# Performance work log

Hardware: AMD Instinct MI355X
Metric: run time of the kernel (lower is better)

## Reference

```python
import jax, jax.numpy as jnp
import numpy as np

HEADS = 8
EPS = 1e-5


def setup_inputs() -> dict:
    key = jax.random.key(0)
    ks = jax.random.split(key, 9)
    B, C, H, W = 4, 256, 128, 128
    s1 = 0.02
    inp = {
        "fmap": jax.random.normal(ks[0], (B, C, H, W), dtype=jnp.float32),
        "g": jnp.ones((C, 1, 1), dtype=jnp.float32),
        "wq1": jax.random.normal(ks[1], (C, C, 1, 1), dtype=jnp.float32) * s1,
        "wq2": jax.random.normal(ks[2], (C, 1, 3, 3), dtype=jnp.float32) * s1,
        "wk1": jax.random.normal(ks[3], (C, C, 1, 1), dtype=jnp.float32) * s1,
        "wk2": jax.random.normal(ks[4], (C, 1, 3, 3), dtype=jnp.float32) * s1,
        "wv1": jax.random.normal(ks[5], (C, C, 1, 1), dtype=jnp.float32) * s1,
        "wv2": jax.random.normal(ks[6], (C, 1, 3, 3), dtype=jnp.float32) * s1,
        "w_out": jax.random.normal(ks[7], (C, C, 1, 1), dtype=jnp.float32) * s1,
    }
    return inp


def _linear_attention(fmap, g, wq1, wq2, wk1, wk2, wv1, wv2, w_out):
    b, C, H, W = fmap.shape
    h = HEADS
    c = C // h          # head dim
    n = H * W           # tokens
    scale = c ** -0.5

    # channel LayerNorm over dim=-3 (C), learned gamma, no bias
    mean = jnp.mean(fmap, axis=1, keepdims=True)
    var = jnp.var(fmap, axis=1, keepdims=True)
    x = (fmap - mean) * jax.lax.rsqrt(var + EPS) * g[None]

    def proj(w1, w2):
        # 1x1 conv (no bias) then 3x3 depthwise conv (groups=C), SAME pad
        y = jnp.einsum('bchw,oc->bohw', x, w1[:, :, 0, 0])
        return jax.lax.conv_general_dilated(
            y, w2, window_strides=(1, 1), padding='SAME',
            dimension_numbers=('NCHW', 'OIHW', 'NCHW'),
            feature_group_count=C)

    q, k, v = proj(wq1, wq2), proj(wk1, wk2), proj(wv1, wv2)

    def to_heads(t):  # [b,C,H,W] -> [b*h, n, c]
        return t.reshape(b, h, c, n).transpose(0, 1, 3, 2).reshape(b * h, n, c)

    q, k, v = to_heads(q), to_heads(k), to_heads(v)

    q = jax.nn.softmax(q, axis=-1) * scale   # softmax over head dim
    k = jax.nn.softmax(k, axis=-2)            # softmax over tokens

    ctx = jnp.einsum('bnd,bne->bde', k, v)    # [b*h, c, c]
    out = jnp.einsum('bnd,bde->bne', q, ctx)  # [b*h, n, c]

    out = out.reshape(b, h, n, c).transpose(0, 1, 3, 2).reshape(b, C, H, W)
    out = jax.nn.silu(out)
    return jnp.einsum('bchw,oc->bohw', out, w_out[:, :, 0, 0])


def reference(fmap, g, wq1, wq2, wk1, wk2, wv1, wv2, w_out):
    return _linear_attention(fmap, g, wq1, wq2, wk1, wk2, wv1, wv2, w_out)
```

## Files before the change

kernel.cpp:

```cpp
#include <hip/hip_runtime.h>
#include <cmath>


#define B 4
#define C 256
#define Hh 128
#define Wd 128
#define HW (Hh*Wd)
#define HEADS 8
#define HD 32
#define OSCALE 256.0f
#define NSP 16

typedef _Float16 half_t;
typedef _Float16 f16x8 __attribute__((ext_vector_type(8)));
typedef float f32x4 __attribute__((ext_vector_type(4)));

__device__ __forceinline__ void gload_lds16(const half_t* g, half_t* l) {
  __builtin_amdgcn_global_load_lds((const __attribute__((address_space(1))) void*)g,
                                   (__attribute__((address_space(3))) void*)l, 16, 0, 0);
}

__global__ __launch_bounds__(256) void wcvt_all(const float* __restrict__ wq1,
                                                const float* __restrict__ wk1,
                                                const float* __restrict__ wv1,
                                                const float* __restrict__ wout,
                                                half_t* __restrict__ Wh,
                                                half_t* __restrict__ Woh,
                                                float* __restrict__ Sk) {
  int i = blockIdx.x * 256 + threadIdx.x;
  if (i < 65536) Wh[i] = (half_t)wq1[i];
  else if (i < 131072) Wh[i] = (half_t)wk1[i - 65536];
  else if (i < 196608) Wh[i] = (half_t)wv1[i - 131072];
  else Woh[i - 196608] = (half_t)wout[i - 196608];
  if (i < B * C) Sk[i] = 0.f;
}

__global__ __launch_bounds__(256) void ln2(const float* __restrict__ fmap,
                                           const float* __restrict__ g,
                                           half_t* __restrict__ Xh) {
  int b = blockIdx.y;
  int lane = threadIdx.x & 63;
  int gq = threadIdx.x >> 6;
  int px = blockIdx.x * 64 + lane;
  __shared__ float gs[C];
  __shared__ float sm1[4][64], sm2[4][64];
  gs[threadIdx.x] = g[threadIdx.x];
  const float* fp = fmap + ((size_t)b * C + gq * 64) * HW + px;
  float vbuf[64];
  float s = 0.f, s2 = 0.f;
#pragma unroll
  for (int j = 0; j < 64; ++j) {
    float v = fp[(size_t)j * HW];
    vbuf[j] = v;
    s += v; s2 = fmaf(v, v, s2);
  }
  sm1[gq][lane] = s; sm2[gq][lane] = s2;
  __syncthreads();
  float st = 0.f, st2 = 0.f;
#pragma unroll
  for (int q = 0; q < 4; ++q) { st += sm1[q][lane]; st2 += sm2[q][lane]; }
  float mean = st * (1.f / C);
  float var = st2 * (1.f / C) - mean * mean;
  float rstd = rsqrtf(var + 1e-5f);
  half_t* xp = Xh + ((size_t)b * HW + px) * 256 + gq * 64;
#pragma unroll
  for (int j0 = 0; j0 < 64; j0 += 8) {
    f16x8 v8;
#pragma unroll
    for (int jj = 0; jj < 8; ++jj)
      v8[jj] = (half_t)((vbuf[j0 + jj] - mean) * rstd * gs[gq * 64 + j0 + jj]);
    *(f16x8*)(xp + j0) = v8;
  }
}

__global__ __launch_bounds__(512) void gemm16r(const half_t* __restrict__ Xh,
                                               const half_t* __restrict__ Wh,
                                               half_t* __restrict__ Yh) {
  __shared__ __align__(16) char smem[65536];
  const int tid = threadIdx.x;
  const int wave = tid >> 6, lane = tid & 63;
  const int lr = lane & 15, lq = lane >> 4;
  const int b = blockIdx.z;
  const int pix0 = blockIdx.x * 128;
  const int m0 = blockIdx.y * 128;
  const int wm = wave >> 1, wn = wave & 1;

  const half_t* xb = Xh + ((size_t)b * HW + pix0) * 256;
  const half_t* wb = Wh + (size_t)m0 * 256;

  f32x4 acc[2][4];
#pragma unroll
  for (int i = 0; i < 2; ++i)
#pragma unroll
    for (int j = 0; j < 4; ++j) { f32x4 z = {0.f, 0.f, 0.f, 0.f}; acc[i][j] = z; }

#define STAGE(kt, s) do {                                                       \
    int r_ = tid >> 2, c_ = tid & 3;                                            \
    int cs_ = c_ ^ ((r_ >> 1) & 3);                                             \
    gload_lds16(xb + (size_t)r_ * 256 + (kt) * 32 + (cs_ << 3),                 \
                (half_t*)(smem + (s) * 16384) + tid * 8);                       \
    gload_lds16(wb + (size_t)r_ * 256 + (kt) * 32 + (cs_ << 3),                 \
                (half_t*)(smem + (s) * 16384 + 8192) + tid * 8);                \
  } while (0)

  STAGE(0, 0);
  STAGE(1, 1);

#pragma unroll
  for (int t = 0; t < 8; ++t) {
    if (t < 6) STAGE(t + 2, (t + 2) & 3);
    if (t < 6)       asm volatile("s_waitcnt vmcnt(4)" ::: "memory");
    else if (t == 6) asm volatile("s_waitcnt vmcnt(2)" ::: "memory");
    else             asm volatile("s_waitcnt vmcnt(0)" ::: "memory");
    __builtin_amdgcn_sched_barrier(0);
    __builtin_amdgcn_s_barrier();
    const char* slot = smem + (t & 3) * 16384;
    f16x8 afr[2], bfr[4];
#pragma unroll
    for (int mf = 0; mf < 2; ++mf) {
      int r = wm * 32 + mf * 16 + lr;
      afr[mf] = *(const f16x8*)(slot + 8192 + r * 64 + ((lq ^ ((r >> 1) & 3)) << 4));
    }
#pragma unroll
    for (int nf = 0; nf < 4; ++nf) {
      int r = wn * 64 + nf * 16 + lr;
      bfr[nf] = *(const f16x8*)(slot + r * 64 + ((lq ^ ((r >> 1) & 3)) << 4));
    }
#pragma unroll
    for (int mf = 0; mf < 2; ++mf)
#pragma unroll
      for (int nf = 0; nf < 4; ++nf)
        acc[mf][nf] = __builtin_amdgcn_mfma_f32_16x16x32_f16(afr[mf], bfr[nf], acc[mf][nf], 0, 0, 0);
  }
#undef STAGE
  asm volatile("s_waitcnt lgkmcnt(0)" ::: "memory");
  __builtin_amdgcn_sched_barrier(0);
  __builtin_amdgcn_s_barrier();

#pragma unroll
  for (int mf = 0; mf < 2; ++mf)
#pragma unroll
    for (int nf = 0; nf < 4; ++nf)
#pragma unroll
      for (int j = 0; j < 4; ++j) {
        int row = wm * 32 + mf * 16 + lq * 4 + j;
        int col = wn * 64 + nf * 16 + lr;
        int byte = row * 256 + ((col * 2) ^ ((row & 7) << 4));
        *(half_t*)(smem + byte) = (half_t)acc[mf][nf][j];
      }
  __syncthreads();
  half_t* dst_base = Yh + (size_t)(m0 >> 8) * ((size_t)B * C * HW)
                     + ((size_t)(b * C + (m0 & 255))) * HW + pix0;
#pragma unroll
  for (int it = 0; it < 4; ++it) {
    int i = it * 512 + tid;
    int row = i >> 4, ch = i & 15;
    int src = row * 256 + ((ch * 16) ^ ((row & 7) << 4));
    *(f16x8*)(dst_base + (size_t)row * HW + ch * 8) = *(const f16x8*)(smem + src);
  }
}

__global__ __launch_bounds__(256) void dw3x3_all(const half_t* __restrict__ Yh,
                                                 const float* __restrict__ wq2,
                                                 const float* __restrict__ wk2,
                                                 const float* __restrict__ wv2,
                                                 half_t* __restrict__ Qh,
                                                 half_t* __restrict__ EK,
                                                 half_t* __restrict__ Vh,
                                                 float* __restrict__ Sk) {
  const size_t SZ = (size_t)B * C * HW;
  int ch = blockIdx.y;
  int ten = ch >> 8;
  int c = ch & 255;
  int b = blockIdx.z;
  int r = threadIdx.x >> 4;
  int cg = threadIdx.x & 15;
  int lane = threadIdx.x & 63;
  int j0 = cg * 8;
  int i = blockIdx.x * 16 + r;
  const half_t* plane = Yh + (size_t)ten * SZ + ((size_t)(b * C + c)) * HW;
  const float* W2 = (ten == 0) ? wq2 : (ten == 1) ? wk2 : wv2;
  half_t wh[9];
#pragma unroll
  for (int k = 0; k < 9; ++k) wh[k] = (half_t)W2[c * 9 + k];
  const int lm1 = (lane - 1) & 63, lp1 = (lane + 1) & 63;
  f16x8 acc8 = {0, 0, 0, 0, 0, 0, 0, 0};
#pragma unroll
  for (int dr = 0; dr < 3; ++dr) {
    int ii = i + dr - 1;
    if (ii < 0 || ii >= Hh) continue;
    uint4 d = *(const uint4*)(plane + ii * Wd + j0);
    unsigned haloL = (unsigned)__shfl((int)d.w, lm1);
    unsigned haloR = (unsigned)__shfl((int)d.x, lp1);
    if (cg == 0)  haloL = 0;
    if (cg == 15) haloR = 0;
    unsigned m0 = __builtin_amdgcn_alignbit(d.x, haloL, 16);
    unsigned m1 = __builtin_amdgcn_alignbit(d.y, d.x, 16);
    unsigned m2 = __builtin_amdgcn_alignbit(d.z, d.y, 16);
    unsigned m3 = __builtin_amdgcn_alignbit(d.w, d.z, 16);
    unsigned m4 = __builtin_amdgcn_alignbit(haloR, d.w, 16);
    uint4 lshu = {m0, m1, m2, m3};
    uint4 rshu = {m1, m2, m3, m4};
    f16x8 cv  = __builtin_bit_cast(f16x8, d);
    f16x8 lsh = __builtin_bit_cast(f16x8, lshu);
    f16x8 rsh = __builtin_bit_cast(f16x8, rshu);
    acc8 += lsh * wh[dr * 3] + cv * wh[dr * 3 + 1] + rsh * wh[dr * 3 + 2];
  }
  size_t off = ((size_t)(b * C + c)) * HW + i * Wd + j0;
  if (ten == 1) {
    f16x8 o8;
    float local = 0.f;
#pragma unroll
    for (int p = 0; p < 8; ++p) {
      float e = expf((float)acc8[p]);
      o8[p] = (half_t)e;
      local += e;
    }
    *(f16x8*)(EK + off) = o8;
    __shared__ float red[256];
    int t = threadIdx.x;
    red[t] = local; __syncthreads();
    for (int st = 128; st > 0; st >>= 1) {
      if (t < st) red[t] += red[t + st];
      __syncthreads();
    }
    if (t == 0) atomicAdd(&Sk[b * C + c], red[0]);
  } else {
    half_t* dst = (ten == 0) ? Qh : Vh;
    *(f16x8*)(dst + off) = acc8;
  }
}

__global__ __launch_bounds__(256) void ctx_mfma(const half_t* __restrict__ EK,
                                                const half_t* __restrict__ V,
                                                float* __restrict__ part) {
  int bh = blockIdx.x, sp = blockIdx.y;
  int wave = threadIdx.x >> 6, lane = threadIdx.x & 63;
  int lr = lane & 15, lq = lane >> 4;
  const size_t base = (size_t)bh * HD * HW;
  const half_t* ekp = EK + base + (size_t)lr * HW;
  const half_t* vp  = V  + base + (size_t)lr * HW;
  f32x4 a00 = {0.f,0.f,0.f,0.f}, a01 = a00, a10 = a00, a11 = a00;
  const int n0w = sp * 1024 + wave * 256 + lq * 8;
#pragma unroll
  for (int ks = 0; ks < 8; ++ks) {
    int n = n0w + ks * 32;
    f16x8 fa0 = *(const f16x8*)(ekp + n);
    f16x8 fa1 = *(const f16x8*)(ekp + (size_t)16 * HW + n);
    f16x8 fb0 = *(const f16x8*)(vp + n);
    f16x8 fb1 = *(const f16x8*)(vp + (size_t)16 * HW + n);
    a00 = __builtin_amdgcn_mfma_f32_16x16x32_f16(fa0, fb0, a00, 0, 0, 0);
    a01 = __builtin_amdgcn_mfma_f32_16x16x32_f16(fa0, fb1, a01, 0, 0, 0);
    a10 = __builtin_amdgcn_mfma_f32_16x16x32_f16(fa1, fb0, a10, 0, 0, 0);
    a11 = __builtin_amdgcn_mfma_f32_16x16x32_f16(fa1, fb1, a11, 0, 0, 0);
  }
  __shared__ float red[4][1024];
#pragma unroll
  for (int j = 0; j < 4; ++j) {
    int dlo = lq * 4 + j;
    red[wave][(dlo)      * 32 + lr]      = a00[j];
    red[wave][(dlo)      * 32 + 16 + lr] = a01[j];
    red[wave][(dlo + 16) * 32 + lr]      = a10[j];
    red[wave][(dlo + 16) * 32 + 16 + lr] = a11[j];
  }
  __syncthreads();
  float* pp = part + ((size_t)sp * 32 + bh) * 1024;
  for (int idx = threadIdx.x; idx < 1024; idx += 256)
    pp[idx] = red[0][idx] + red[1][idx] + red[2][idx] + red[3][idx];
}

__global__ __launch_bounds__(256) void ctxred(const float* __restrict__ part,
                                              const float* __restrict__ Sk,
                                              half_t* __restrict__ ctxh) {
  int bh = blockIdx.x;
  int t = threadIdx.x;
  for (int idx = t; idx < 1024; idx += 256) {
    int d = idx >> 5, e = idx & 31;
    float s = 0.f;
#pragma unroll
    for (int sp = 0; sp < NSP; ++sp) s += part[((size_t)sp * 32 + bh) * 1024 + idx];
    ctxh[(size_t)bh * 1024 + e * 32 + d] = (half_t)(s / Sk[bh * HD + d]);
  }
}

__global__ __launch_bounds__(256) void attn6b(const half_t* __restrict__ Qh,
                                              const half_t* __restrict__ ctxh,
                                              const half_t* __restrict__ Woh,
                                              float* __restrict__ outp) {
  const int b = blockIdx.y;
  const int lane = threadIdx.x & 63;
  const int w = threadIdx.x >> 6;
  const int lr = lane & 15, lq = lane >> 4;
  const int px0 = blockIdx.x * 64;
  const int px = px0 + w * 16 + lr;
  __shared__ __align__(16) char osm[64 * 512];

  {
    const int pxl_base = w * 16 + lq * 4;
    const half_t* cb = ctxh + ((size_t)b * HEADS) * 1024;
    f16x8 cf0 = *(const f16x8*)(cb + (lr)      * 32 + lq * 8);
    f16x8 cf1 = *(const f16x8*)(cb + (16 + lr) * 32 + lq * 8);
#pragma unroll
    for (int h = 0; h < HEADS; ++h) {
      f16x8 nf0, nf1;
      if (h < HEADS - 1) {
        const half_t* nb = cb + (size_t)(h + 1) * 1024;
        nf0 = *(const f16x8*)(nb + (lr)      * 32 + lq * 8);
        nf1 = *(const f16x8*)(nb + (16 + lr) * 32 + lq * 8);
      }
      const half_t* qp = Qh + ((size_t)(b * C + h * HD + lq * 8)) * HW + px;
      float ev[8];
      float psum = 0.f;
#pragma unroll
      for (int j = 0; j < 8; ++j) {
        ev[j] = expf((float)qp[(size_t)j * HW]);
        psum += ev[j];
      }
      float s = psum;
      s += __shfl_xor(s, 16, 64);
      s += __shfl_xor(s, 32, 64);
      float inv = 0.1767766952966369f / s;
      f16x8 pa;
#pragma unroll
      for (int j = 0; j < 8; ++j) pa[j] = (half_t)(ev[j] * inv);

      f32x4 z = {0.f, 0.f, 0.f, 0.f};
      f32x4 a0 = __builtin_amdgcn_mfma_f32_16x16x32_f16(pa, cf0, z, 0, 0, 0);
      f32x4 a1 = __builtin_amdgcn_mfma_f32_16x16x32_f16(pa, cf1, z, 0, 0, 0);
#pragma unroll
      for (int eh = 0; eh < 2; ++eh) {
        f32x4 a = eh ? a1 : a0;
        int cc = h * 32 + eh * 16 + lr;
#pragma unroll
        for (int j = 0; j < 4; ++j) {
          int pxl = pxl_base + j;
          float v = a[j];
          float sg = 1.f / (1.f + expf(-v));
          int byte = pxl * 512 + ((cc * 2) ^ ((pxl & 7) << 4));
          *(half_t*)(osm + byte) = (half_t)(v * sg * OSCALE);
        }
      }
      cf0 = nf0; cf1 = nf1;
    }
  }
  __syncthreads();

  f32x4 acc[4][4];
#pragma unroll
  for (int i = 0; i < 4; ++i)
#pragma unroll
    for (int j = 0; j < 4; ++j) { f32x4 z = {0.f, 0.f, 0.f, 0.f}; acc[i][j] = z; }

  const half_t* wbase = Woh + ((size_t)(w * 64 + lr)) * 256 + lq * 8;
#pragma unroll
  for (int k0 = 0; k0 < 256; k0 += 32) {
    f16x8 afr[4], bfr[4];
#pragma unroll
    for (int mf = 0; mf < 4; ++mf)
      afr[mf] = *(const f16x8*)(wbase + (size_t)(mf * 16) * 256 + k0);
#pragma unroll
    for (int nf = 0; nf < 4; ++nf) {
      int r = nf * 16 + lr;
      bfr[nf] = *(const f16x8*)(osm + r * 512 + ((k0 * 2 + lq * 16) ^ ((r & 7) << 4)));
    }
#pragma unroll
    for (int mf = 0; mf < 4; ++mf)
#pragma unroll
      for (int nf = 0; nf < 4; ++nf)
        acc[mf][nf] = __builtin_amdgcn_mfma_f32_16x16x32_f16(afr[mf], bfr[nf], acc[mf][nf], 0, 0, 0);
  }

#pragma unroll
  for (int mf = 0; mf < 4; ++mf) {
    int oc = w * 64 + mf * 16 + lq * 4;
#pragma unroll
    for (int nf = 0; nf < 4; ++nf) {
      float* dst = outp + ((size_t)(b * C + oc)) * HW + px0 + nf * 16 + lr;
#pragma unroll
      for (int j = 0; j < 4; ++j)
        dst[(size_t)j * HW] = acc[mf][nf][j] * (1.0f / OSCALE);
    }
  }
}

extern "C" void kernel_launch(void* const* d_in, const int* in_sizes, int n_in,
                              void* d_out, int out_size, void* d_ws, size_t ws_size,
                              hipStream_t stream) {
  const float* fmap = (const float*)d_in[0];
  const float* g    = (const float*)d_in[1];
  const float* wq1  = (const float*)d_in[2];
  const float* wq2  = (const float*)d_in[3];
  const float* wk1  = (const float*)d_in[4];
  const float* wk2  = (const float*)d_in[5];
  const float* wv1  = (const float*)d_in[6];
  const float* wv2  = (const float*)d_in[7];
  const float* wout = (const float*)d_in[8];
  float* out = (float*)d_out;
  char* ws = (char*)d_ws;

  const size_t SZ = (size_t)B * C * HW;
  const size_t Mi = (size_t)1 << 20;
  half_t* Xh   = (half_t*)(ws);
  half_t* Yh   = (half_t*)(ws + 32 * Mi);
  half_t* Qh   = (half_t*)(ws + 128 * Mi);
  half_t* EK   = (half_t*)(ws);
  half_t* Vh   = (half_t*)out;
  float*  part = (float*)(ws + 96 * Mi);
  float*  Sk   = (float*)(ws + 160 * Mi);
  half_t* ctxh = (half_t*)(ws + 100 * Mi);
  half_t* Wh   = (half_t*)(ws + 192 * Mi);
  half_t* Woh  = (half_t*)(ws + 192 * Mi + 512 * 1024);

  wcvt_all<<<dim3(1024), 256, 0, stream>>>(wq1, wk1, wv1, wout, Wh, Woh, Sk);

  ln2<<<dim3(HW / 64, B), 256, 0, stream>>>(fmap, g, Xh);

  gemm16r<<<dim3(HW / 128, 6, B), 512, 0, stream>>>(Xh, Wh, Yh);

  dw3x3_all<<<dim3(Hh / 16, 3 * C, B), 256, 0, stream>>>(Yh, wq2, wk2, wv2,
                                                         Qh, EK, Vh, Sk);

  ctx_mfma<<<dim3(HEADS * B, NSP), 256, 0, stream>>>(EK, Vh, part);
  ctxred<<<dim3(32), 256, 0, stream>>>(part, Sk, ctxh);

  attn6b<<<dim3(HW / 64, B), 256, 0, stream>>>(Qh, ctxh, Woh, out);
}
```

Before: 169.5 us.

## Stage weight tile once in LDS and read activations directly from global

```diff
diff --git a/kernel.cpp b/kernel.cpp
--- a/kernel.cpp
+++ b/kernel.cpp
@@ -74,7 +74,7 @@
   }
 }
 
-__global__ __launch_bounds__(512) void gemm16r(const half_t* __restrict__ Xh,
+__global__ __launch_bounds__(512) void gemm16s(const half_t* __restrict__ Xh,
                                                const half_t* __restrict__ Wh,
                                                half_t* __restrict__ Yh) {
   __shared__ __align__(16) char smem[65536];
@@ -86,8 +86,17 @@
   const int m0 = blockIdx.y * 128;
   const int wm = wave >> 1, wn = wave & 1;
 
-  const half_t* xb = Xh + ((size_t)b * HW + pix0) * 256;
   const half_t* wb = Wh + (size_t)m0 * 256;
+#pragma unroll
+  for (int it = 0; it < 8; ++it) {
+    int e = it * 512 + tid;
+    int m = e >> 5, ch = e & 31;
+    int chg = ch ^ (m & 7);
+    gload_lds16(wb + (size_t)m * 256 + chg * 8, (half_t*)smem + e * 8);
+  }
+  __syncthreads();
+
+  const half_t* xb = Xh + ((size_t)b * HW + pix0 + wn * 64 + lr) * 256 + lq * 8;
 
   f32x4 acc[2][4];
 #pragma unroll
@@ -95,37 +104,18 @@
 #pragma unroll
     for (int j = 0; j < 4; ++j) { f32x4 z = {0.f, 0.f, 0.f, 0.f}; acc[i][j] = z; }
 
-#define STAGE(kt, s) do {                                                       \
-    int r_ = tid >> 2, c_ = tid & 3;                                            \
-    int cs_ = c_ ^ ((r_ >> 1) & 3);                                             \
-    gload_lds16(xb + (size_t)r_ * 256 + (kt) * 32 + (cs_ << 3),                 \
-                (half_t*)(smem + (s) * 16384) + tid * 8);                       \
-    gload_lds16(wb + (size_t)r_ * 256 + (kt) * 32 + (cs_ << 3),                 \
-                (half_t*)(smem + (s) * 16384 + 8192) + tid * 8);                \
-  } while (0)
-
-  STAGE(0, 0);
-  STAGE(1, 1);
-
-#pragma unroll
-  for (int t = 0; t < 8; ++t) {
-    if (t < 6) STAGE(t + 2, (t + 2) & 3);
-    if (t < 6)       asm volatile("s_waitcnt vmcnt(4)" ::: "memory");
-    else if (t == 6) asm volatile("s_waitcnt vmcnt(2)" ::: "memory");
-    else             asm volatile("s_waitcnt vmcnt(0)" ::: "memory");
-    __builtin_amdgcn_sched_barrier(0);
-    __builtin_amdgcn_s_barrier();
-    const char* slot = smem + (t & 3) * 16384;
-    f16x8 afr[2], bfr[4];
+#pragma unroll
+  for (int ks = 0; ks < 8; ++ks) {
+    f16x8 bfr[4];
+#pragma unroll
+    for (int nf = 0; nf < 4; ++nf)
+      bfr[nf] = *(const f16x8*)(xb + (size_t)(nf * 16) * 256 + ks * 32);
+    f16x8 afr[2];
 #pragma unroll
     for (int mf = 0; mf < 2; ++mf) {
-      int r = wm * 32 + mf * 16 + lr;
-      afr[mf] = *(const f16x8*)(slot + 8192 + r * 64 + ((lq ^ ((r >> 1) & 3)) << 4));
-    }
-#pragma unroll
-    for (int nf = 0; nf < 4; ++nf) {
-      int r = wn * 64 + nf * 16 + lr;
-      bfr[nf] = *(const f16x8*)(slot + r * 64 + ((lq ^ ((r >> 1) & 3)) << 4));
+      int m = wm * 32 + mf * 16 + lr;
+      int ch = (ks * 4 + lq) ^ (m & 7);
+      afr[mf] = *(const f16x8*)(smem + m * 512 + ch * 16);
     }
 #pragma unroll
     for (int mf = 0; mf < 2; ++mf)
@@ -133,10 +123,7 @@
       for (int nf = 0; nf < 4; ++nf)
         acc[mf][nf] = __builtin_amdgcn_mfma_f32_16x16x32_f16(afr[mf], bfr[nf], acc[mf][nf], 0, 0, 0);
   }
-#undef STAGE
-  asm volatile("s_waitcnt lgkmcnt(0)" ::: "memory");
-  __builtin_amdgcn_sched_barrier(0);
-  __builtin_amdgcn_s_barrier();
+  __syncthreads();
 
 #pragma unroll
   for (int mf = 0; mf < 2; ++mf)
@@ -416,7 +403,7 @@
 
   ln2<<<dim3(HW / 64, B), 256, 0, stream>>>(fmap, g, Xh);
 
-  gemm16r<<<dim3(HW / 128, 6, B), 512, 0, stream>>>(Xh, Wh, Yh);
+  gemm16s<<<dim3(HW / 128, 6, B), 512, 0, stream>>>(Xh, Wh, Yh);
 
   dw3x3_all<<<dim3(Hh / 16, 3 * C, B), 256, 0, stream>>>(Yh, wq2, wk2, wv2,
                                                          Qh, EK, Vh, Sk);
```

Measured after the change: 226.7 us. 33.8% more time.
